# Kernel tuning notes

Hardware: AMD Instinct MI355X
Metric: run time of the kernel (lower is better)

## Reference

```python
import jax, jax.numpy as jnp
import numpy as np

N = 8_388_608          # sequence length (timesteps)
DT = 300.0             # dt_seconds
BOUNDS = {
    "R_env": (1e-3, 1e-1),
    "R_int": (1e-3, 1e-1),
    "R_vent": (1e-3, 1e-1),
    "C_air": (1e5, 1e7),
}

def _scaled(w, name):
    lo, hi = BOUNDS[name]
    return lo + jax.nn.sigmoid(w) * (hi - lo)

def setup_inputs() -> dict:
    key = jax.random.key(0)
    k1, = jax.random.split(key, 1)
    return {
        "T_init": jnp.asarray(20.0, jnp.float32),
        "inputs": jax.random.normal(k1, (N, 4), jnp.float32),
        "w_R_env": jnp.zeros((), jnp.float32),
        "w_R_int": jnp.zeros((), jnp.float32),
        "w_R_vent": jnp.zeros((), jnp.float32),
        "w_C_air": jnp.zeros((), jnp.float32),
    }

def reference(T_init, inputs, w_R_env, w_R_int, w_R_vent, w_C_air):
    # physical parameters via bounded sigmoid (R_int computed in the original
    # but unused in the forward dynamics)
    R_env = _scaled(w_R_env, "R_env")
    R_vent = _scaled(w_R_vent, "R_vent")
    C_air = _scaled(w_C_air, "C_air")
    inv_R_eq = 1.0 / R_env + 1.0 / R_vent

    # Explicit Euler: T_{t+1} = T_t + DT*((T_out_t - T_t)*inv_R_eq + Q_tot_t)/C_air
    #              = a * T_t + b_t  with constant a and precomputed drive b.
    a = 1.0 - DT * inv_R_eq / C_air
    x = inputs[:-1]                                  # (N-1, 4) driving data
    b = DT * (x[:, 0] * inv_R_eq + x[:, 1] + x[:, 2] + x[:, 3]) / C_air  # (N-1,)

    def step(T, b_t):
        T_next = a * T + b_t
        return T_next, T_next

    _, Ts = jax.lax.scan(step, T_init, b)            # (N-1,)
    return jnp.concatenate([T_init[None], Ts])       # (N,)
```

## Files before the change

### kernel.cpp

```cpp
#include <hip/hip_runtime.h>
#include <hip/hip_bf16.h>

#define BLOCK 256
#define LT 32
#define LB (BLOCK * LT)
#define K2THREADS 1024
#define SWZ(i) ((i) + ((i) >> 5))

static __device__ __forceinline__ float sigmoidf_(float w) {
    return 1.0f / (1.0f + expf(-w));
}

struct Params { float a; float invReq; float scale; float T0; };

static __device__ __forceinline__ Params compute_params(const float* T_init, const float* wRe,
                                                        const float* wRv, const float* wC) {
    const float DT = 300.0f;
    float R_env  = 0.001f + sigmoidf_(*wRe) * (0.1f - 0.001f);
    float R_vent = 0.001f + sigmoidf_(*wRv) * (0.1f - 0.001f);
    float C_air  = 1.0e5f + sigmoidf_(*wC) * (1.0e7f - 1.0e5f);
    Params p;
    p.invReq = 1.0f / R_env + 1.0f / R_vent;
    p.a      = 1.0f - DT * p.invReq / C_air;
    p.scale  = DT / C_air;
    p.T0     = *T_init;
    return p;
}

template<int NT>
static __device__ __forceinline__ void ks_scan(float& m, float& s, float* sm, float* ss, int t) {
    sm[t] = m; ss[t] = s;
    __syncthreads();
    for (int d = 1; d < NT; d <<= 1) {
        float pm = 1.0f, ps = 0.0f;
        bool act = (t >= d);
        if (act) { pm = sm[t - d]; ps = ss[t - d]; }
        __syncthreads();
        if (act) { s = fmaf(m, ps, s); m *= pm; sm[t] = m; ss[t] = s; }
        __syncthreads();
    }
}

template<bool HAVE_B>
__global__ __launch_bounds__(BLOCK) void k1_partials(
    const float4* __restrict__ x, const float* __restrict__ T_init,
    const float* __restrict__ wRe, const float* __restrict__ wRv, const float* __restrict__ wC,
    float* __restrict__ b_out, float* __restrict__ partials, int M)
{
    __shared__ float lds_b[LB + LB / 32];
    __shared__ float sm[BLOCK], ss[BLOCK];
    Params p = compute_params(T_init, wRe, wRv, wC);
    const int base = blockIdx.x * LB;
    const int t = threadIdx.x;

    for (int j = t; j < LB; j += BLOCK) {
        int g = base + j;
        float b = 0.0f;
        if (g < M) {
            float4 r = x[g];
            b = p.scale * (fmaf(r.x, p.invReq, r.y) + r.z + r.w);
            if (HAVE_B) b_out[g] = b;
        }
        lds_b[SWZ(j)] = b;
    }
    __syncthreads();

    float s = 0.0f;
    const int lb = t * (LT + 1);
    #pragma unroll
    for (int i = 0; i < LT; ++i) s = fmaf(p.a, s, lds_b[lb + i]);

    float a2 = p.a * p.a, a4 = a2 * a2, a8 = a4 * a4, a16 = a8 * a8, a32 = a16 * a16;
    float m = a32;
    ks_scan<BLOCK>(m, s, sm, ss, t);
    if (t == BLOCK - 1) partials[blockIdx.x] = s;
}

__global__ __launch_bounds__(K2THREADS) void k2_scan(
    const float* __restrict__ partials, float* __restrict__ carries,
    const float* __restrict__ T_init, const float* __restrict__ wRe,
    const float* __restrict__ wRv, const float* __restrict__ wC, int nblocks)
{
    __shared__ float sm[K2THREADS], ss[K2THREADS];
    Params p = compute_params(T_init, wRe, wRv, wC);
    float aB = p.a;
    #pragma unroll
    for (int i = 0; i < 13; ++i) aB *= aB;
    const int t = threadIdx.x;
    float m = aB;
    float s = (t < nblocks) ? partials[t] : 0.0f;
    ks_scan<K2THREADS>(m, s, sm, ss, t);
    if (t < nblocks) {
        float g = (t == 0) ? p.T0 : fmaf(sm[t - 1], p.T0, ss[t - 1]);
        carries[t] = g;
    }
}

template<bool HAVE_B>
__global__ __launch_bounds__(BLOCK) void k3_emit(
    const float4* __restrict__ x, const float* __restrict__ b_in,
    const float* __restrict__ carries, const float* __restrict__ T_init,
    const float* __restrict__ wRe, const float* __restrict__ wRv, const float* __restrict__ wC,
    float* __restrict__ out, int M)
{
    __shared__ float lds_b[LB + LB / 32];
    __shared__ float sm[BLOCK], ss[BLOCK];
    Params p = compute_params(T_init, wRe, wRv, wC);
    const int base = blockIdx.x * LB;
    const int t = threadIdx.x;

    for (int j = t; j < LB; j += BLOCK) {
        int g = base + j;
        float b = 0.0f;
        if (g < M) {
            if (HAVE_B) {
                b = b_in[g];
            } else {
                float4 r = x[g];
                b = p.scale * (fmaf(r.x, p.invReq, r.y) + r.z + r.w);
            }
        }
        lds_b[SWZ(j)] = b;
    }
    __syncthreads();

    float s = 0.0f;
    const int lb = t * (LT + 1);
    #pragma unroll
    for (int i = 0; i < LT; ++i) s = fmaf(p.a, s, lds_b[lb + i]);

    float a2 = p.a * p.a, a4 = a2 * a2, a8 = a4 * a4, a16 = a8 * a8, a32 = a16 * a16;
    float m = a32;
    ks_scan<BLOCK>(m, s, sm, ss, t);

    float me = 1.0f, se = 0.0f;
    if (t > 0) { me = sm[t - 1]; se = ss[t - 1]; }
    float G = carries[blockIdx.x];
    float T = fmaf(me, G, se);

    #pragma unroll
    for (int i = 0; i < LT; ++i) {
        T = fmaf(p.a, T, lds_b[lb + i]);
        lds_b[lb + i] = T;
    }
    __syncthreads();

    for (int j = t; j < LB; j += BLOCK) {
        int g = base + j;
        if (g < M) out[g + 1] = lds_b[SWZ(j)];
    }
    if (blockIdx.x == 0 && t == 0) out[0] = p.T0;
}

extern "C" void kernel_launch(void* const* d_in, const int* in_sizes, int n_in,
                              void* d_out, int out_size, void* d_ws, size_t ws_size,
                              hipStream_t stream)
{
    const float*  T_init = (const float*)d_in[0];
    const float4* x      = (const float4*)d_in[1];
    const float*  wRe    = (const float*)d_in[2];
    const float*  wRv    = (const float*)d_in[4];
    const float*  wC     = (const float*)d_in[5];
    float* out = (float*)d_out;

    const int N = out_size;
    const int M = N - 1;
    const int nblocks = (M + LB - 1) / LB;

    float* partials = (float*)d_ws;
    float* carries  = partials + 1024;
    float* b_buf    = carries + 1024;
    const size_t need_b = 8192 + (size_t)M * sizeof(float);
    const bool have_b = (ws_size >= need_b);

    if (have_b) {
        k1_partials<true ><<<nblocks, BLOCK, 0, stream>>>(x, T_init, wRe, wRv, wC, b_buf, partials, M);
    } else {
        k1_partials<false><<<nblocks, BLOCK, 0, stream>>>(x, T_init, wRe, wRv, wC, nullptr, partials, M);
    }
    k2_scan<<<1, K2THREADS, 0, stream>>>(partials, carries, T_init, wRe, wRv, wC, nblocks);
    if (have_b) {
        k3_emit<true ><<<nblocks, BLOCK, 0, stream>>>(x, b_buf, carries, T_init, wRe, wRv, wC, out, M);
    } else {
        k3_emit<false><<<nblocks, BLOCK, 0, stream>>>(x, nullptr, carries, T_init, wRe, wRv, wC, out, M);
    }
}
```

Baseline: 233.6 us.

## Fuse three-pass scan into one cooperative kernel with grid syncs

Merges the partials, block-carry scan and emit kernels into a single cooperative launch that keeps each block's drive values in LDS across two grid-wide barriers. Block 0 scans the per-block partials with four values per thread. This removes the intermediate b buffer write and re-read plus the extra kernel launches. The cost is relying on cooperative residency: 1024 blocks each using about 35KB of LDS must all be co-resident, otherwise the launch fails. Grid syncs also add latency.

```diff
diff --git a/kernel.cpp b/kernel.cpp
--- a/kernel.cpp
+++ b/kernel.cpp
@@ -1,10 +1,12 @@
 #include <hip/hip_runtime.h>
 #include <hip/hip_bf16.h>
+#include <hip/hip_cooperative_groups.h>
+
+namespace cg = cooperative_groups;
 
 #define BLOCK 256
 #define LT 32
 #define LB (BLOCK * LT)
-#define K2THREADS 1024
 #define SWZ(i) ((i) + ((i) >> 5))
 
 static __device__ __forceinline__ float sigmoidf_(float w) {
@@ -41,14 +43,15 @@
     }
 }
 
-template<bool HAVE_B>
-__global__ __launch_bounds__(BLOCK) void k1_partials(
+__global__ __launch_bounds__(BLOCK, 4) void fused_scan(
     const float4* __restrict__ x, const float* __restrict__ T_init,
     const float* __restrict__ wRe, const float* __restrict__ wRv, const float* __restrict__ wC,
-    float* __restrict__ b_out, float* __restrict__ partials, int M)
+    float* __restrict__ out, float* __restrict__ partials, float* __restrict__ carries, int M)
 {
     __shared__ float lds_b[LB + LB / 32];
     __shared__ float sm[BLOCK], ss[BLOCK];
+    cg::grid_group grid = cg::this_grid();
+
     Params p = compute_params(T_init, wRe, wRv, wC);
     const int base = blockIdx.x * LB;
     const int t = threadIdx.x;
@@ -59,66 +62,6 @@
         if (g < M) {
             float4 r = x[g];
             b = p.scale * (fmaf(r.x, p.invReq, r.y) + r.z + r.w);
-            if (HAVE_B) b_out[g] = b;
-        }
-        lds_b[SWZ(j)] = b;
-    }
-    __syncthreads();
-
-    float s = 0.0f;
-    const int lb = t * (LT + 1);
-    #pragma unroll
-    for (int i = 0; i < LT; ++i) s = fmaf(p.a, s, lds_b[lb + i]);
-
-    float a2 = p.a * p.a, a4 = a2 * a2, a8 = a4 * a4, a16 = a8 * a8, a32 = a16 * a16;
-    float m = a32;
-    ks_scan<BLOCK>(m, s, sm, ss, t);
-    if (t == BLOCK - 1) partials[blockIdx.x] = s;
-}
-
-__global__ __launch_bounds__(K2THREADS) void k2_scan(
-    const float* __restrict__ partials, float* __restrict__ carries,
-    const float* __restrict__ T_init, const float* __restrict__ wRe,
-    const float* __restrict__ wRv, const float* __restrict__ wC, int nblocks)
-{
-    __shared__ float sm[K2THREADS], ss[K2THREADS];
-    Params p = compute_params(T_init, wRe, wRv, wC);
-    float aB = p.a;
-    #pragma unroll
-    for (int i = 0; i < 13; ++i) aB *= aB;
-    const int t = threadIdx.x;
-    float m = aB;
-    float s = (t < nblocks) ? partials[t] : 0.0f;
-    ks_scan<K2THREADS>(m, s, sm, ss, t);
-    if (t < nblocks) {
-        float g = (t == 0) ? p.T0 : fmaf(sm[t - 1], p.T0, ss[t - 1]);
-        carries[t] = g;
-    }
-}
-
-template<bool HAVE_B>
-__global__ __launch_bounds__(BLOCK) void k3_emit(
-    const float4* __restrict__ x, const float* __restrict__ b_in,
-    const float* __restrict__ carries, const float* __restrict__ T_init,
-    const float* __restrict__ wRe, const float* __restrict__ wRv, const float* __restrict__ wC,
-    float* __restrict__ out, int M)
-{
-    __shared__ float lds_b[LB + LB / 32];
-    __shared__ float sm[BLOCK], ss[BLOCK];
-    Params p = compute_params(T_init, wRe, wRv, wC);
-    const int base = blockIdx.x * LB;
-    const int t = threadIdx.x;
-
-    for (int j = t; j < LB; j += BLOCK) {
-        int g = base + j;
-        float b = 0.0f;
-        if (g < M) {
-            if (HAVE_B) {
-                b = b_in[g];
-            } else {
-                float4 r = x[g];
-                b = p.scale * (fmaf(r.x, p.invReq, r.y) + r.z + r.w);
-            }
         }
         lds_b[SWZ(j)] = b;
     }
@@ -135,9 +78,41 @@
 
     float me = 1.0f, se = 0.0f;
     if (t > 0) { me = sm[t - 1]; se = ss[t - 1]; }
+    if (t == BLOCK - 1) partials[blockIdx.x] = s;
+
+    grid.sync();
+
+    if (blockIdx.x == 0) {
+        float aB = p.a;
+        #pragma unroll
+        for (int i = 0; i < 13; ++i) aB *= aB;
+        const int nb = gridDim.x;
+        float vals[4];
+        float mm = 1.0f, s2 = 0.0f;
+        #pragma unroll
+        for (int k = 0; k < 4; ++k) {
+            int j = t * 4 + k;
+            float pj = (j < nb) ? partials[j] : 0.0f;
+            vals[k] = pj;
+            s2 = fmaf(aB, s2, pj);
+            mm *= aB;
+        }
+        ks_scan<BLOCK>(mm, s2, sm, ss, t);
+        float Me = 1.0f, Se = 0.0f;
+        if (t > 0) { Me = sm[t - 1]; Se = ss[t - 1]; }
+        float G = fmaf(Me, p.T0, Se);
+        #pragma unroll
+        for (int k = 0; k < 4; ++k) {
+            int j = t * 4 + k;
+            if (j < nb) carries[j] = G;
+            G = fmaf(aB, G, vals[k]);
+        }
+    }
+
+    grid.sync();
+
     float G = carries[blockIdx.x];
     float T = fmaf(me, G, se);
-
     #pragma unroll
     for (int i = 0; i < LT; ++i) {
         T = fmaf(p.a, T, lds_b[lb + i]);
@@ -163,25 +138,17 @@
     const float*  wC     = (const float*)d_in[5];
     float* out = (float*)d_out;
 
-    const int N = out_size;
-    const int M = N - 1;
-    const int nblocks = (M + LB - 1) / LB;
+    int N = out_size;
+    int M = N - 1;
+    int nblocks = (M + LB - 1) / LB;
 
     float* partials = (float*)d_ws;
     float* carries  = partials + 1024;
-    float* b_buf    = carries + 1024;
-    const size_t need_b = 8192 + (size_t)M * sizeof(float);
-    const bool have_b = (ws_size >= need_b);
 
-    if (have_b) {
-        k1_partials<true ><<<nblocks, BLOCK, 0, stream>>>(x, T_init, wRe, wRv, wC, b_buf, partials, M);
-    } else {
-        k1_partials<false><<<nblocks, BLOCK, 0, stream>>>(x, T_init, wRe, wRv, wC, nullptr, partials, M);
-    }
-    k2_scan<<<1, K2THREADS, 0, stream>>>(partials, carries, T_init, wRe, wRv, wC, nblocks);
-    if (have_b) {
-        k3_emit<true ><<<nblocks, BLOCK, 0, stream>>>(x, b_buf, carries, T_init, wRe, wRv, wC, out, M);
-    } else {
-        k3_emit<false><<<nblocks, BLOCK, 0, stream>>>(x, nullptr, carries, T_init, wRe, wRv, wC, out, M);
-    }
+    void* args[] = {
+        (void*)&x, (void*)&T_init, (void*)&wRe, (void*)&wRv, (void*)&wC,
+        (void*)&out, (void*)&partials, (void*)&carries, (void*)&M
+    };
+    hipLaunchCooperativeKernel((const void*)fused_scan, dim3(nblocks), dim3(BLOCK),
+                               args, 0, stream);
 }
```

Result: slower. 400.6 us (+71.5%).
